# Performance work log

Measured on AMD Instinct MI355X. Metric: run time of the kernel, lower is better.

Reference implementation:

```python
import jax, jax.numpy as jnp
import numpy as np

RADIUS = 0.1
NSAMPLE = 32


def setup_inputs() -> dict:
    key = jax.random.key(0)
    k1, k2, k3 = jax.random.split(key, 3)
    B, N, P, C = 2, 16384, 4096, 64
    xyz = jax.random.uniform(k1, (B, N, 3), dtype=jnp.float32)
    new_xyz = jax.random.uniform(k2, (B, P, 3), dtype=jnp.float32)
    features = jax.random.normal(k3, (B, C, N), dtype=jnp.float32)
    return {"xyz": xyz, "new_xyz": new_xyz, "features": features}


def _ball_query(xyz, new_xyz, radius, nsample):
    """Return (B, npoint, nsample) int32 indices of the first `nsample` points
    (in original order) within `radius` of each query center. Slots beyond the
    number of valid neighbors are padded with the first valid index (0 if none),
    matching the standard PointNet++ CUDA ball_query semantics."""
    N = xyz.shape[1]
    # squared distances [B, P, N]
    d2 = jnp.sum((new_xyz[:, :, None, :] - xyz[:, None, :, :]) ** 2, axis=-1)
    in_ball = d2 < (radius * radius)
    # score = point index if in ball, else N (sentinel); smallest nsample scores
    # are the first nsample in-ball indices in original order.
    score = jnp.where(in_ball, jnp.arange(N, dtype=jnp.int32), jnp.int32(N))
    neg_topk, _ = jax.lax.top_k(-score, nsample)  # largest of -score == smallest score
    idx = -neg_topk  # [B, P, nsample], ascending
    first = idx[..., :1]
    idx = jnp.where(idx >= N, first, idx)  # pad invalid slots with first valid
    idx = jnp.where(idx >= N, 0, idx)      # no neighbor at all -> 0
    return idx


def _group(features, idx):
    """features (B, C, N), idx (B, P, S) -> (B, C, P, S)"""
    return jax.vmap(lambda f, i: f[:, i])(features, idx)


def reference(xyz, new_xyz, features):
    idx = _ball_query(xyz, new_xyz, RADIUS, NSAMPLE)          # (B, P, S)
    xyz_t = jnp.transpose(xyz, (0, 2, 1))                      # (B, 3, N)
    grouped_xyz = _group(xyz_t, idx)                           # (B, 3, P, S)
    grouped_xyz = grouped_xyz - jnp.transpose(new_xyz, (0, 2, 1))[..., None]
    grouped_features = _group(features, idx)                   # (B, C, P, S)
    new_features = jnp.concatenate([grouped_xyz, grouped_features], axis=1)
    return new_features
```

## Files before the change

kernel.cpp:

```cpp
#include <hip/hip_runtime.h>
#include <limits.h>

#define BB 2
#define NN 16384
#define PP 4096
#define CC 64
#define SS 32
#define R2 0.01f
#define OUTCH (3 + CC)
#define GRES 10
#define NCELL 1000
#define TILE 128
#define BINBLK 128

__device__ __forceinline__ int cell_of(float v) {
  int q = (int)(v * 10.0f);
  return q < 0 ? 0 : (q > GRES - 1 ? GRES - 1 : q);
}
__device__ __forceinline__ int cell_clamp_floor(float v) {
  int q = (int)floorf(v * 10.0f);
  return q < 0 ? 0 : (q > GRES - 1 ? GRES - 1 : q);
}

__global__ __launch_bounds__(256) void transpose_feat_kernel(
    const float* __restrict__ feat, float* __restrict__ featT,
    int* __restrict__ zeroRegion) {
  __shared__ float tile[64][65];
  const int n0 = blockIdx.x * 64;
  const int b = blockIdx.y;
  const int jn = threadIdx.x & 63;
  const int g4 = threadIdx.x >> 6;

  if (blockIdx.x == 0 && blockIdx.y == 0) {
    for (int k = threadIdx.x; k < 2 * BB * NCELL + 8; k += 256) zeroRegion[k] = 0;
  }

  const float* fb = feat + (size_t)b * CC * NN;
#pragma unroll
  for (int k = 0; k < 16; ++k) {
    const int c = g4 * 16 + k;
    tile[c][jn] = fb[(size_t)c * NN + n0 + jn];
  }
  __syncthreads();
  float* ft = featT + ((size_t)b * NN + n0) * CC;
#pragma unroll
  for (int k = 0; k < 16; ++k) {
    const int j = g4 * 16 + k;
    ft[(size_t)j * CC + jn] = tile[jn][j];
  }
}

__global__ __launch_bounds__(256) void bin_all_kernel(
    const float* __restrict__ xyz, int* __restrict__ histG,
    int* __restrict__ fillG, int* __restrict__ doneG,
    int* __restrict__ cellStartG, float4* __restrict__ sorted4) {
  __shared__ int cstart[NCELL];
  __shared__ int wsum[4];
  const int blk = blockIdx.x;
  const int b = blk >> 6;
  const int t = threadIdx.x;
  const int lane = t & 63;
  const int w = t >> 6;
  const int i = (blk & 63) * 256 + t;

  const float* p = xyz + ((size_t)b * NN + i) * 3;
  const float x = p[0], y = p[1], z = p[2];
  const int c = (cell_of(z) * GRES + cell_of(y)) * GRES + cell_of(x);
  atomicAdd(histG + b * NCELL + c, 1);

  __threadfence();
  __syncthreads();
  if (t == 0) {
    atomicAdd(doneG, 1);
    while (__hip_atomic_load(doneG, __ATOMIC_ACQUIRE,
                             __HIP_MEMORY_SCOPE_AGENT) < BINBLK) {
    }
  }
  __syncthreads();

  int v0 = 0, v1 = 0, v2 = 0, v3 = 0, s = 0;
  if (t < 250) {
    const int base = b * NCELL + t * 4;
    v0 = __hip_atomic_load(histG + base + 0, __ATOMIC_RELAXED, __HIP_MEMORY_SCOPE_AGENT);
    v1 = __hip_atomic_load(histG + base + 1, __ATOMIC_RELAXED, __HIP_MEMORY_SCOPE_AGENT);
    v2 = __hip_atomic_load(histG + base + 2, __ATOMIC_RELAXED, __HIP_MEMORY_SCOPE_AGENT);
    v3 = __hip_atomic_load(histG + base + 3, __ATOMIC_RELAXED, __HIP_MEMORY_SCOPE_AGENT);
    s = v0 + v1 + v2 + v3;
  }
  int incl = s;
#pragma unroll
  for (int d = 1; d < 64; d <<= 1) {
    const int u = __shfl_up(incl, d);
    if (lane >= d) incl += u;
  }
  if (lane == 63) wsum[w] = incl;
  __syncthreads();
  int pre = 0;
#pragma unroll
  for (int k = 0; k < 4; ++k) pre += (k < w) ? wsum[k] : 0;
  if (t < 250) {
    int run = pre + incl - s;
    cstart[t * 4 + 0] = run; run += v0;
    cstart[t * 4 + 1] = run; run += v1;
    cstart[t * 4 + 2] = run; run += v2;
    cstart[t * 4 + 3] = run;
  }
  __syncthreads();

  if ((blk & 63) == 0) {
    if (t < 250) {
#pragma unroll
      for (int k = 0; k < 4; ++k)
        cellStartG[b * 1001 + t * 4 + k] = cstart[t * 4 + k];
    }
    if (t == 0) cellStartG[b * 1001 + NCELL] = NN;
  }

  const int r = atomicAdd(fillG + b * NCELL + c, 1);
  const int pos = cstart[c] + r;
  float4 vv;
  vv.x = x; vv.y = y; vv.z = z; vv.w = __int_as_float(i);
  sorted4[(size_t)b * NN + pos] = vv;
}

__global__ __launch_bounds__(256) void query_group_kernel(
    const float4* __restrict__ sorted4, const int* __restrict__ cellStart,
    const float* __restrict__ new_xyz, const float* __restrict__ xyz,
    const float* __restrict__ featT, float* __restrict__ out) {
#pragma clang fp contract(off)
  __shared__ float smem[TILE * 65];
  __shared__ int idxsm[TILE];
  const int widx = threadIdx.x >> 6;
  const int lane = threadIdx.x & 63;
  const int wave = blockIdx.x * 4 + widx;
  const int b = wave >> 12;
  unsigned* bm = (unsigned*)smem + widx * 576;
  int* myout = idxsm + widx * SS;

  const float cx = new_xyz[wave * 3 + 0];
  const float cy = new_xyz[wave * 3 + 1];
  const float cz = new_xyz[wave * 3 + 2];
  const float4* __restrict__ sb = sorted4 + (size_t)b * NN;
  const int* __restrict__ csb = cellStart + b * 1001;

#pragma unroll
  for (int k = 0; k < 9; ++k) bm[k * 64 + lane] = 0;

  const float mg = 0.1f + 1e-5f;
  const int loy = cell_clamp_floor(cy - mg), hiy = cell_clamp_floor(cy + mg);
  const int loz = cell_clamp_floor(cz - mg), hiz = cell_clamp_floor(cz + mg);
  const int ny = hiy - loy + 1;
  const int nz = hiz - loz + 1;
  const int nr = nz * ny;

  int s_l = 0, len_l = 0;
  if (lane < nr) {
    int zi, yi;
    if (ny == 1) { zi = lane; yi = 0; }
    else if (ny == 2) { zi = lane >> 1; yi = lane & 1; }
    else { zi = (lane * 11) >> 5; yi = lane - zi * 3; }
    const int zc = loz + zi, yc = loy + yi;
    const float y0 = yc * 0.1f, z0 = zc * 0.1f;
    const float dymin = fmaxf(fmaxf(y0 - cy, cy - (y0 + 0.1f)), 0.0f);
    const float dzmin = fmaxf(fmaxf(z0 - cz, cz - (z0 + 0.1f)), 0.0f);
    const float rem = mg * mg - dymin * dymin - dzmin * dzmin;
    if (rem > 0.0f) {
      const float dxa = sqrtf(rem) * 1.0000002f + 1e-7f;
      const int lxr = cell_clamp_floor(cx - dxa);
      const int hxr = cell_clamp_floor(cx + dxa);
      const int c0 = (zc * GRES + yc) * GRES + lxr;
      s_l = csb[c0];
      len_l = csb[c0 + (hxr - lxr + 1)] - s_l;
    }
  }
  int incl = len_l;
#pragma unroll
  for (int d = 1; d <= 8; d <<= 1) {
    const int v = __shfl_up(incl, d);
    if (lane >= d) incl += v;
  }
  const int T = __shfl(incl, nr - 1);
  const int Lx = incl - len_l;

  int Lk[9], Sk[9];
#pragma unroll
  for (int k = 0; k < 9; ++k) {
    Lk[k] = __shfl(Lx, k);
    Sk[k] = __shfl(s_l, k);
  }

  auto flat_load = [&](int g) -> float4 {
    int L = Lk[0], S = Sk[0];
#pragma unroll
    for (int k = 1; k < 9; ++k) {
      const bool cge = g >= Lk[k];
      L = cge ? Lk[k] : L;
      S = cge ? Sk[k] : S;
    }
    return sb[S + (g - L)];
  };

  const int nIt = (T + 63) >> 6;
  float4 cur = {};
  if (lane < T) cur = flat_load(lane);
  for (int it = 0; it < nIt; ++it) {
    float4 nxt = cur;
    const int gn = (it + 1) * 64 + lane;
    if (gn < T) nxt = flat_load(gn);
    const int g = it * 64 + lane;
    if (g < T) {
      const float dx = cx - cur.x;
      const float dy = cy - cur.y;
      const float dz = cz - cur.z;
      const float a = dx * dx + dy * dy;
      const float d2 = a + dz * dz;
      if (d2 < R2) {
        const int orig = __float_as_int(cur.w);
        const int wi = orig >> 5;
        atomicOr(&bm[(wi >> 3) * 9 + (wi & 7)], 1u << (orig & 31));
      }
    }
    cur = nxt;
  }
  __threadfence_block();

  unsigned wv[8];
  int c = 0;
  int fi = INT_MAX;
#pragma unroll
  for (int k = 0; k < 8; ++k) {
    wv[k] = bm[lane * 9 + k];
    c += (int)__popc(wv[k]);
    if (fi == INT_MAX && wv[k])
      fi = lane * 256 + k * 32 + (int)__builtin_ctz(wv[k]);
  }

  int incl2 = c;
#pragma unroll
  for (int d = 1; d < 64; d <<= 1) {
    const int t = __shfl_up(incl2, d);
    if (lane >= d) incl2 += t;
  }
  const int E = incl2 - c;
  const int total = __shfl(incl2, 63);

  const unsigned long long nb = __ballot(c > 0);
  int fc = 0;
  if (nb) fc = __shfl(fi, (int)__builtin_ctzll(nb));

  int s = E;
  if (s < SS) {
#pragma unroll
    for (int k = 0; k < 8; ++k) {
      unsigned ww = wv[k];
      while (ww && s < SS) {
        const int bpos = (int)__builtin_ctz(ww);
        ww &= ww - 1;
        myout[s++] = lane * 256 + k * 32 + bpos;
      }
      if (s >= SS) break;
    }
  }
  for (int s2 = total + lane; s2 < SS; s2 += 64) myout[s2] = fc;

  __syncthreads();

  const int base = blockIdx.x * TILE;
  const int t = threadIdx.x;
  const size_t PS = (size_t)PP * SS;

  const float4* ftb = (const float4*)(featT + (size_t)b * NN * CC);
#pragma unroll
  for (int k = 0; k < 8; ++k) {
    const int u = k * 256 + t;
    const int r = u >> 4;
    const int q = u & 15;
    const int v = idxsm[r];
    const float4 val = ftb[(size_t)v * 16 + q];
    float* dst = &smem[r * 65 + q * 4];
    dst[0] = val.x; dst[1] = val.y; dst[2] = val.z; dst[3] = val.w;
  }
  __syncthreads();

  if (t < TILE) {
    const int g = base + t;
    const int v = idxsm[t];
    const int p = (g >> 5) & (PP - 1);
    const float* xr = xyz + ((size_t)b * NN + v) * 3;
    const float* cr = new_xyz + (size_t)(b * PP + p) * 3;
    const size_t ob = (size_t)b * OUTCH * PS + ((size_t)g & (PS - 1));
    out[ob + 0 * PS] = xr[0] - cr[0];
    out[ob + 1 * PS] = xr[1] - cr[1];
    out[ob + 2 * PS] = xr[2] - cr[2];
  }

  float* ob3 = out + (size_t)b * OUTCH * PS + 3 * PS + ((size_t)base & (PS - 1));
#pragma unroll
  for (int k = 0; k < 32; ++k) {
    const int u = k * 256 + t;
    const int c2 = u >> 7;
    const int r = u & 127;
    ob3[(size_t)c2 * PS + r] = smem[r * 65 + c2];
  }
}

extern "C" void kernel_launch(void* const* d_in, const int* in_sizes, int n_in,
                              void* d_out, int out_size, void* d_ws, size_t ws_size,
                              hipStream_t stream) {
  const float* xyz = (const float*)d_in[0];
  const float* new_xyz = (const float*)d_in[1];
  const float* feat = (const float*)d_in[2];
  float* out = (float*)d_out;

  float* featT = (float*)d_ws;
  char* p = (char*)d_ws + (size_t)BB * NN * CC * sizeof(float);
  float4* sorted4 = (float4*)p;
  p += (size_t)BB * NN * sizeof(float4);
  int* cellStart = (int*)p;
  p += (size_t)BB * 1001 * sizeof(int);
  int* hist = (int*)p;
  int* fill = hist + BB * NCELL;
  int* done = fill + BB * NCELL;

  transpose_feat_kernel<<<dim3(NN / 64, BB), 256, 0, stream>>>(feat, featT, hist);
  bin_all_kernel<<<BINBLK, 256, 0, stream>>>(xyz, hist, fill, done, cellStart,
                                             sorted4);
  query_group_kernel<<<(BB * PP) / 4, 256, 0, stream>>>(sorted4, cellStart,
                                                        new_xyz, xyz, featT, out);
}
```

Measured before the change: 64.07 us.

## Split fused ball-query/group kernel into two kernels via scratch indices in output

Splits the combined query+group kernel into a ball query kernel that writes 16-bit neighbor indices into the output buffer (channel 0 region) and a separate group kernel that reads them back and gathers features. This lets the query kernel run with small LDS (bitmasks only), and gives the gather kernel its own occupancy profile, at the cost of an extra launch and an index round-trip through global memory. Output channel 0 region is overwritten later by the group kernel, which relies on each block reading its own slots before writing xyz.

```diff
diff --git a/kernel.cpp b/kernel.cpp
--- a/kernel.cpp
+++ b/kernel.cpp
@@ -123,19 +123,22 @@
   sorted4[(size_t)b * NN + pos] = vv;
 }
 
-__global__ __launch_bounds__(256) void query_group_kernel(
+__global__ __launch_bounds__(256) void ball_query_kernel(
     const float4* __restrict__ sorted4, const int* __restrict__ cellStart,
-    const float* __restrict__ new_xyz, const float* __restrict__ xyz,
-    const float* __restrict__ featT, float* __restrict__ out) {
+    const float* __restrict__ new_xyz, float* out) {
 #pragma clang fp contract(off)
-  __shared__ float smem[TILE * 65];
-  __shared__ int idxsm[TILE];
+  __shared__ unsigned bmAll[4 * 576];
   const int widx = threadIdx.x >> 6;
   const int lane = threadIdx.x & 63;
   const int wave = blockIdx.x * 4 + widx;
   const int b = wave >> 12;
-  unsigned* bm = (unsigned*)smem + widx * 576;
-  int* myout = idxsm + widx * SS;
+  unsigned* bm = bmAll + widx * 576;
+
+  const int base = blockIdx.x * TILE;
+  const size_t PS = (size_t)PP * SS;
+  ushort* slotU =
+      (ushort*)(out + (size_t)b * OUTCH * PS + ((size_t)base & (PS - 1)));
+  ushort* myout = slotU + widx * SS;
 
   const float cx = new_xyz[wave * 3 + 0];
   const float cy = new_xyz[wave * 3 + 1];
@@ -256,18 +259,28 @@
       while (ww && s < SS) {
         const int bpos = (int)__builtin_ctz(ww);
         ww &= ww - 1;
-        myout[s++] = lane * 256 + k * 32 + bpos;
+        myout[s++] = (ushort)(lane * 256 + k * 32 + bpos);
       }
       if (s >= SS) break;
     }
   }
-  for (int s2 = total + lane; s2 < SS; s2 += 64) myout[s2] = fc;
-
-  __syncthreads();
-
+  for (int s2 = total + lane; s2 < SS; s2 += 64) myout[s2] = (ushort)fc;
+}
+
+__global__ __launch_bounds__(256) void group_kernel_t(
+    const float* __restrict__ xyz, const float* __restrict__ new_xyz,
+    const float* __restrict__ featT, float* out) {
+  __shared__ float lds[TILE * 65];
+  __shared__ int idxsm[TILE];
   const int base = blockIdx.x * TILE;
+  const int b = base >> 17;
   const int t = threadIdx.x;
   const size_t PS = (size_t)PP * SS;
+
+  const ushort* slotU =
+      (const ushort*)(out + (size_t)b * OUTCH * PS + ((size_t)base & (PS - 1)));
+  if (t < TILE) idxsm[t] = (int)slotU[t];
+  __syncthreads();
 
   const float4* ftb = (const float4*)(featT + (size_t)b * NN * CC);
 #pragma unroll
@@ -277,7 +290,7 @@
     const int q = u & 15;
     const int v = idxsm[r];
     const float4 val = ftb[(size_t)v * 16 + q];
-    float* dst = &smem[r * 65 + q * 4];
+    float* dst = &lds[r * 65 + q * 4];
     dst[0] = val.x; dst[1] = val.y; dst[2] = val.z; dst[3] = val.w;
   }
   __syncthreads();
@@ -300,7 +313,7 @@
     const int u = k * 256 + t;
     const int c2 = u >> 7;
     const int r = u & 127;
-    ob3[(size_t)c2 * PS + r] = smem[r * 65 + c2];
+    ob3[(size_t)c2 * PS + r] = lds[r * 65 + c2];
   }
 }
 
@@ -325,6 +338,8 @@
   transpose_feat_kernel<<<dim3(NN / 64, BB), 256, 0, stream>>>(feat, featT, hist);
   bin_all_kernel<<<BINBLK, 256, 0, stream>>>(xyz, hist, fill, done, cellStart,
                                              sorted4);
-  query_group_kernel<<<(BB * PP) / 4, 256, 0, stream>>>(sorted4, cellStart,
-                                                        new_xyz, xyz, featT, out);
-}
+  ball_query_kernel<<<(BB * PP) / 4, 256, 0, stream>>>(sorted4, cellStart,
+                                                       new_xyz, out);
+  group_kernel_t<<<(BB * PP * SS) / TILE, 256, 0, stream>>>(xyz, new_xyz, featT,
+                                                            out);
+}
```

Measured after the change: 91.88 us. 1.43x slower.
